# Kernel optimization log

Hardware: AMD Instinct MI355X
Metric: run time of the kernel (lower is better)

Reference implementation:

```python
import jax, jax.numpy as jnp
import numpy as np

GROUPS = 8   # channels // group_size with group_size=8 for C=64
EPS = 1e-5


def group_norm_qc(x0, x1, gamma, beta):
    """LatticeGroupNorm: stats computed jointly over both cosets per (batch, group)."""
    B, C, H, W = x0.shape
    g = GROUPS
    xg = jnp.concatenate([x0.reshape(B, g, -1), x1.reshape(B, g, -1)], axis=-1)
    mean = xg.mean(axis=-1).reshape(B, g, 1, 1, 1)
    var = xg.var(axis=-1).reshape(B, g, 1, 1, 1)
    inv = jax.lax.rsqrt(var + EPS)
    ga = gamma[None, :, None, None]
    be = beta[None, :, None, None]

    def norm(x):
        xr = x.reshape(B, g, C // g, H, W)
        return ((xr - mean) * inv).reshape(B, C, H, W) * ga + be

    return norm(x0), norm(x1)


def qc_conv(x0, x1, w_center, w_corner, bias):
    """Quincunx LatticePad+LatticeConvolution with stencil
    [(0,0),(2,0),(0,2),(2,2),(1,1)], center (1,1).
    w_center: [O,I] tap (1,1) (same-coset 1x1).
    w_corner: [O,I,2,2] taps (0,0),(2,0),(0,2),(2,2) (cross-coset 2x2).
    Pad keeps output cosets the same size as inputs ('same' lattice conv)."""
    dn = ('NCHW', 'OIHW', 'NCHW')

    def c1(x):
        return jnp.einsum('oi,bihw->bohw', w_center, x)

    def c2(x, pad):
        return jax.lax.conv_general_dilated(x, w_corner, (1, 1), pad,
                                            dimension_numbers=dn)

    b = bias[None, :, None, None]
    # coset0 output gathers coset1 at (i-1+a, j-1+b) -> pad top/left
    out0 = c1(x0) + c2(x1, ((1, 0), (1, 0))) + b
    # coset1 output gathers coset0 at (i+a, j+b) -> pad bottom/right
    out1 = c1(x1) + c2(x0, ((0, 1), (0, 1))) + b
    return out0, out1


def setup_inputs() -> dict:
    key = jax.random.key(0)
    ks = jax.random.split(key, 10)
    B, C, H, W = 2, 64, 256, 256
    s = 0.05
    return {
        'x0': jax.random.normal(ks[0], (B, C, H, W), jnp.float32),
        'x1': jax.random.normal(ks[1], (B, C, H, W), jnp.float32),
        'g1': jnp.ones((C,), jnp.float32),
        'b1': jnp.zeros((C,), jnp.float32),
        'w1_center': jax.random.normal(ks[2], (C, C), jnp.float32) * s,
        'w1_corner': jax.random.normal(ks[3], (C, C, 2, 2), jnp.float32) * s,
        'bias1': jax.random.normal(ks[4], (C,), jnp.float32) * s,
        'g2': jnp.ones((C,), jnp.float32),
        'b2': jnp.zeros((C,), jnp.float32),
        'w2_center': jax.random.normal(ks[5], (C, C), jnp.float32) * s,
        'w2_corner': jax.random.normal(ks[6], (C, C, 2, 2), jnp.float32) * s,
        'bias2': jax.random.normal(ks[7], (C,), jnp.float32) * s,
        'w_skip': jax.random.normal(ks[8], (C, C), jnp.float32) * s,
        'bias_skip': jax.random.normal(ks[9], (C,), jnp.float32) * s,
        'g_skip': jnp.ones((C,), jnp.float32),
        'beta_skip': jnp.zeros((C,), jnp.float32),
    }


def reference(x0, x1, g1, b1, w1_center, w1_corner, bias1,
              g2, b2, w2_center, w2_corner, bias2,
              w_skip, bias_skip, g_skip, beta_skip):
    # conv path: GN -> ReLU -> pad+conv -> GN -> ReLU -> pad+conv
    h0, h1 = group_norm_qc(x0, x1, g1, b1)
    h0, h1 = jax.nn.relu(h0), jax.nn.relu(h1)
    h0, h1 = qc_conv(h0, h1, w1_center, w1_corner, bias1)
    h0, h1 = group_norm_qc(h0, h1, g2, b2)
    h0, h1 = jax.nn.relu(h0), jax.nn.relu(h1)
    h0, h1 = qc_conv(h0, h1, w2_center, w2_corner, bias2)
    # skip path: 1x1 lattice conv (stencil [(0,0)]) -> GN
    bsk = bias_skip[None, :, None, None]
    s0 = jnp.einsum('oi,bihw->bohw', w_skip, x0) + bsk
    s1 = jnp.einsum('oi,bihw->bohw', w_skip, x1) + bsk
    s0, s1 = group_norm_qc(s0, s1, g_skip, beta_skip)
    # residual add; stack the two cosets as leading axis for a single output
    return jnp.stack([h0 + s0, h1 + s1])
```

## Files before the change

kernel.cpp:

```cpp
#include <hip/hip_runtime.h>

typedef __attribute__((ext_vector_type(8))) __bf16 bf16x8;
typedef __attribute__((ext_vector_type(4))) __bf16 bf16x4;
typedef __attribute__((ext_vector_type(4))) float f32x4;

#define MFMA16(a,b,c) __builtin_amdgcn_mfma_f32_16x16x32_bf16(a,b,c,0,0,0)

static constexpr int HW = 65536;
static constexpr int WD = 256;
static constexpr int NB = 2;
static constexpr double INV_N = 1.0 / 1048576.0;
static constexpr float EPSV = 1e-5f;

static constexpr size_t OFF_P1  = 0;
static constexpr size_t OFF_P2  = 131072;
static constexpr size_t OFF_A1  = 200704;
static constexpr size_t OFF_A2  = OFF_A1 + 40960;
static constexpr size_t OFF_XT  = OFF_A2 + 40960;
static constexpr size_t SZ_T    = (size_t)2 * NB * HW * 64 * 2;
static constexpr size_t OFF_S   = OFF_XT + SZ_T;
static constexpr size_t OFF_H   = OFF_S + SZ_T;

__global__ __launch_bounds__(256) void K1(
    const float* __restrict__ x0, const float* __restrict__ x1,
    const float* __restrict__ wskip, const float* __restrict__ bskip,
    const float* __restrict__ wc1, const float* __restrict__ wk1,
    const float* __restrict__ wc2, const float* __restrict__ wk2,
    __bf16* __restrict__ xt, __bf16* __restrict__ sout,
    __bf16* __restrict__ A1, __bf16* __restrict__ A2, float* __restrict__ p1) {
  const int bx = blockIdx.x;
  const int t = threadIdx.x;

  if (bx >= 1024) {
    const int stage = bx - 1024;
    const float* wc = stage ? wc2 : wc1;
    const float* wk = stage ? wk2 : wk1;
    __bf16* A = stage ? A2 : A1;
    for (int idx = t; idx < 64 * 320; idx += 256) {
      int o = idx / 320, k = idx - o * 320;
      float v;
      if (k < 64) v = wc[o * 64 + k];
      else {
        int tp = (k - 64) >> 6;
        int c = k & 63;
        v = wk[(o * 64 + c) * 4 + tp];
      }
      A[idx] = (__bf16)v;
    }
    return;
  }

  const int row = bx & 255;
  const int b   = (bx >> 8) & 1;
  const int co  = bx >> 9;
  const float* x = co ? x1 : x0;
  __shared__ __attribute__((aligned(16))) __bf16 tile[256 * 72];
  __shared__ float redp[256];
  __shared__ float reds[32];
  const int wv = t >> 6, lane = t & 63;

  const float* xbase = x + (size_t)b * 64 * HW + (size_t)row * WD + t;
  __bf16* xtbase = xt + (((size_t)(co * NB + b) * HW) + (size_t)row * WD + t) * 64;

  float gsum[8], gsq[8];
#pragma unroll
  for (int g = 0; g < 8; ++g) { gsum[g] = 0.f; gsq[g] = 0.f; }
#pragma unroll
  for (int cg = 0; cg < 8; ++cg) {
    float f[8];
#pragma unroll
    for (int j = 0; j < 8; ++j) f[j] = xbase[(size_t)(cg * 8 + j) * HW];
    bf16x8 v;
#pragma unroll
    for (int j = 0; j < 8; ++j) {
      v[j] = (__bf16)f[j];
      gsum[cg] += f[j];
      gsq[cg] = fmaf(f[j], f[j], gsq[cg]);
    }
    *(bf16x8*)&tile[t * 72 + cg * 8] = v;
    *(bf16x8*)&xtbase[cg * 8] = v;
  }
#pragma unroll
  for (int g = 0; g < 8; ++g) {
#pragma unroll
    for (int m = 1; m < 16; m <<= 1) {
      gsum[g] += __shfl_xor(gsum[g], m, 64);
      gsq[g]  += __shfl_xor(gsq[g], m, 64);
    }
  }
  {
    const int q0 = lane >> 4;
    if ((lane & 15) == 0) {
#pragma unroll
      for (int g = 0; g < 8; ++g) {
        redp[(wv * 4 + q0) * 16 + g] = gsum[g];
        redp[(wv * 4 + q0) * 16 + 8 + g] = gsq[g];
      }
    }
  }
  __syncthreads();

  const int ln = lane & 15, q = lane >> 4;
  const int ch0 = wv * 16 + q * 4;
  bf16x8 a0, a1;
#pragma unroll
  for (int j = 0; j < 8; ++j) {
    a0[j] = (__bf16)wskip[(wv * 16 + ln) * 64 + q * 8 + j];
    a1[j] = (__bf16)wskip[(wv * 16 + ln) * 64 + 32 + q * 8 + j];
  }
  float bia[4];
#pragma unroll
  for (int r = 0; r < 4; ++r) bia[r] = bskip[ch0 + r];

  float ssum = 0.f, ssq = 0.f;
  for (int n = 0; n < 16; ++n) {
    f32x4 acc = {0.f, 0.f, 0.f, 0.f};
    bf16x8 b0 = *(const bf16x8*)&tile[(n * 16 + ln) * 72 + q * 8];
    bf16x8 b1 = *(const bf16x8*)&tile[(n * 16 + ln) * 72 + 32 + q * 8];
    acc = MFMA16(a0, b0, acc);
    acc = MFMA16(a1, b1, acc);
    bf16x4 sv;
    float v[4];
#pragma unroll
    for (int r = 0; r < 4; ++r) {
      v[r] = acc[r] + bia[r];
      ssum += v[r];
      ssq = fmaf(v[r], v[r], ssq);
      sv[r] = (__bf16)v[r];
    }
    size_t sb = ((size_t)(co * NB + b) * 4096 + row * 16 + n) * 1024 + (wv * 4 + q) * 64 + ln * 4;
    *(bf16x4*)&sout[sb] = sv;
  }
#pragma unroll
  for (int m = 1; m < 16; m <<= 1) {
    ssum += __shfl_xor(ssum, m, 64);
    ssq  += __shfl_xor(ssq, m, 64);
  }
  if ((lane & 15) == 0) {
    reds[wv * 4 + q] = ssum;
    reds[16 + wv * 4 + q] = ssq;
  }

  __syncthreads();
  if (t < 32) {
    float val;
    if (t < 16) {
      val = 0.f;
#pragma unroll
      for (int k = 0; k < 16; ++k) val += redp[k * 16 + t];
    } else {
      int kind = (t >> 3) & 1, g = t & 7;
      int wvv = g >> 1, qp = g & 1;
      val = reds[kind * 16 + wvv * 4 + qp * 2] + reds[kind * 16 + wvv * 4 + qp * 2 + 1];
    }
    const int bf1 = (co * 2 + b) * 256 + row;
    p1[(size_t)bf1 * 32 + t] = val;
  }
}

__global__ __launch_bounds__(256) void K2(
    const __bf16* __restrict__ xt, const __bf16* __restrict__ A1,
    const float* __restrict__ p1, const float* __restrict__ g1, const float* __restrict__ be1,
    const float* __restrict__ bias1,
    __bf16* __restrict__ h, float* __restrict__ p2) {
  const int blk = ((blockIdx.x & 7) << 6) | (blockIdx.x >> 3);
  const int tx = blk & 15, ty = blk >> 4;
  const int b = blockIdx.y;
  const int y0p = ty * 8, x0p = tx * 16;
  __shared__ __attribute__((aligned(16))) __bf16 tl[2][153 * 72];
  __shared__ double redn[16];
  __shared__ float sc[64], sh[64];
  __shared__ float lst[16];
  const int t = threadIdx.x;

  {
    const int col = t >> 4, sub = t & 15;
    double v = 0.0;
    for (int j = sub; j < 512; j += 16) {
      int cc = j >> 8, rr = j & 255;
      v += (double)p1[((size_t)(cc * 2 + b) * 256 + rr) * 32 + col];
    }
    v += __shfl_xor(v, 1, 64);
    v += __shfl_xor(v, 2, 64);
    v += __shfl_xor(v, 4, 64);
    v += __shfl_xor(v, 8, 64);
    if (sub == 0) redn[col] = v;
  }
  if (t < 16) lst[t] = 0.f;
  __syncthreads();
  if (t < 64) {
    int g = t >> 3;
    double mean = redn[g] * INV_N;
    double var  = redn[8 + g] * INV_N - mean * mean;
    float inv = rsqrtf((float)var + EPSV);
    float s_ = inv * g1[t];
    sc[t] = s_;
    sh[t] = be1[t] - (float)mean * s_;
  }
  __syncthreads();

#pragma unroll
  for (int i = 0; i < 10; ++i) {
    int u = t + i * 256;
    if (u < 2 * 153 * 8) {
      int cs = u / 1224;
      int rr = u - cs * 1224;
      int px = rr >> 3, cg = rr & 7;
      int ly = px / 17, lx = px - ly * 17;
      int gy = y0p + ly - cs, gx = x0p + lx - cs;
      bf16x8 v;
#pragma unroll
      for (int j = 0; j < 8; ++j) v[j] = (__bf16)0.f;
      if ((unsigned)gy < 256u && (unsigned)gx < 256u) {
        bf16x8 raw = *(const bf16x8*)&xt[(((size_t)(cs * NB + b) * WD + gy) * WD + gx) * 64 + cg * 8];
#pragma unroll
        for (int j = 0; j < 8; ++j) {
          float f = fmaf((float)raw[j], sc[cg * 8 + j], sh[cg * 8 + j]);
          v[j] = (__bf16)fmaxf(f, 0.f);
        }
      }
      *(bf16x8*)&tl[cs][px * 72 + cg * 8] = v;
    }
  }
  __syncthreads();

  const int wv = t >> 6, lane = t & 63, ln = lane & 15, q = lane >> 4;
  const int co = wv & 1, mh = wv >> 1;
  const int q8 = q * 8;
  bf16x8 af[2][10];
#pragma unroll
  for (int m = 0; m < 2; ++m)
#pragma unroll
    for (int kk = 0; kk < 10; ++kk)
      af[m][kk] = *(const bf16x8*)&A1[(mh * 32 + m * 16 + ln) * 320 + kk * 32 + q8];

  f32x4 acc[8][2];
#pragma unroll
  for (int n = 0; n < 8; ++n)
#pragma unroll
    for (int m = 0; m < 2; ++m) acc[n][m] = (f32x4){0.f, 0.f, 0.f, 0.f};

  const __bf16* tc = tl[co];
  const __bf16* to = tl[1 - co];
#pragma unroll
  for (int n = 0; n < 8; ++n) {
    const int cpix = co ? ((n + 1) * 17 + ln + 1) : (n * 17 + ln);
    const int tb = n * 17 + ln;
    const __bf16* pc = tc + cpix * 72 + q8;
    const __bf16* p0 = to + tb * 72 + q8;
    const __bf16* p1p = to + (tb + 1) * 72 + q8;
    const __bf16* p2p = to + (tb + 17) * 72 + q8;
    const __bf16* p3 = to + (tb + 18) * 72 + q8;
    bf16x8 bb;
    bb = *(const bf16x8*)pc;         acc[n][0]=MFMA16(af[0][0],bb,acc[n][0]); acc[n][1]=MFMA16(af[1][0],bb,acc[n][1]);
    bb = *(const bf16x8*)(pc + 32);  acc[n][0]=MFMA16(af[0][1],bb,acc[n][0]); acc[n][1]=MFMA16(af[1][1],bb,acc[n][1]);
    bb = *(const bf16x8*)p0;         acc[n][0]=MFMA16(af[0][2],bb,acc[n][0]); acc[n][1]=MFMA16(af[1][2],bb,acc[n][1]);
    bb = *(const bf16x8*)(p0 + 32);  acc[n][0]=MFMA16(af[0][3],bb,acc[n][0]); acc[n][1]=MFMA16(af[1][3],bb,acc[n][1]);
    bb = *(const bf16x8*)p1p;        acc[n][0]=MFMA16(af[0][4],bb,acc[n][0]); acc[n][1]=MFMA16(af[1][4],bb,acc[n][1]);
    bb = *(const bf16x8*)(p1p + 32); acc[n][0]=MFMA16(af[0][5],bb,acc[n][0]); acc[n][1]=MFMA16(af[1][5],bb,acc[n][1]);
    bb = *(const bf16x8*)p2p;        acc[n][0]=MFMA16(af[0][6],bb,acc[n][0]); acc[n][1]=MFMA16(af[1][6],bb,acc[n][1]);
    bb = *(const bf16x8*)(p2p + 32); acc[n][0]=MFMA16(af[0][7],bb,acc[n][0]); acc[n][1]=MFMA16(af[1][7],bb,acc[n][1]);
    bb = *(const bf16x8*)p3;         acc[n][0]=MFMA16(af[0][8],bb,acc[n][0]); acc[n][1]=MFMA16(af[1][8],bb,acc[n][1]);
    bb = *(const bf16x8*)(p3 + 32);  acc[n][0]=MFMA16(af[0][9],bb,acc[n][0]); acc[n][1]=MFMA16(af[1][9],bb,acc[n][1]);
  }

  __syncthreads();

  float s2s[2] = {0.f, 0.f}, s2q[2] = {0.f, 0.f};
  float bia[2][4];
#pragma unroll
  for (int m = 0; m < 2; ++m)
#pragma unroll
    for (int r = 0; r < 4; ++r) bia[m][r] = bias1[mh * 32 + m * 16 + q * 4 + r];

#pragma unroll
  for (int n = 0; n < 8; ++n)
#pragma unroll
    for (int m = 0; m < 2; ++m) {
      bf16x4 hv;
#pragma unroll
      for (int r = 0; r < 4; ++r) {
        float v = acc[n][m][r] + bia[m][r];
        s2s[m] += v;
        s2q[m] = fmaf(v, v, s2q[m]);
        hv[r] = (__bf16)v;
      }
      *(bf16x4*)&tl[co][(n * 16 + ln) * 72 + mh * 32 + m * 16 + q * 4] = hv;
    }

#pragma unroll
  for (int m = 0; m < 2; ++m) {
    float a_ = s2s[m], c_ = s2q[m];
#pragma unroll
    for (int mk = 1; mk < 32; mk <<= 1) {
      a_ += __shfl_xor(a_, mk, 64);
      c_ += __shfl_xor(c_, mk, 64);
    }
    if ((lane & 31) == 0) {
      int g = mh * 4 + m * 2 + (q >> 1);
      atomicAdd(&lst[g], a_);
      atomicAdd(&lst[8 + g], c_);
    }
  }
  __syncthreads();

#pragma unroll
  for (int i = 0; i < 8; ++i) {
    int co2 = i >> 2;
    int idx = (i & 3) * 256 + t;
    int px = idx >> 3, chunk = idx & 7;
    int gy = y0p + (px >> 4), gx = x0p + (px & 15);
    bf16x8 vv = *(const bf16x8*)&tl[co2][px * 72 + chunk * 8];
    *(bf16x8*)&h[(((size_t)(co2 * NB + b) * WD + gy) * WD + gx) * 64 + chunk * 8] = vv;
  }

  if (t < 16) p2[((size_t)b * 512 + blockIdx.x) * 16 + t] = lst[t];
}

__global__ __launch_bounds__(256) void K3(
    const __bf16* __restrict__ hin, const __bf16* __restrict__ A2,
    const float* __restrict__ p2, const float* __restrict__ p1,
    const float* __restrict__ g2, const float* __restrict__ be2, const float* __restrict__ bias2,
    const float* __restrict__ gsk, const float* __restrict__ besk,
    const __bf16* __restrict__ sin_, float* __restrict__ out) {
  const int blk = ((blockIdx.x & 7) << 6) | (blockIdx.x >> 3);
  const int tx = blk & 15, ty = blk >> 4;
  const int b = blockIdx.y;
  const int y0p = ty * 8, x0p = tx * 16;
  __shared__ __attribute__((aligned(16))) __bf16 tl[2][153 * 72];
  __shared__ double redn[32];
  __shared__ float sc2[64], sh2[64], scS[64], shS[64];
  const int t = threadIdx.x;

  {
    const int col = t >> 3, sub = t & 7;
    double v = 0.0;
    if (col < 16) {
      for (int j = sub; j < 512; j += 8)
        v += (double)p2[((size_t)b * 512 + j) * 16 + col];
    } else {
      for (int j = sub; j < 512; j += 8) {
        int cc = j >> 8, rr = j & 255;
        v += (double)p1[((size_t)(cc * 2 + b) * 256 + rr) * 32 + col];
      }
    }
    v += __shfl_xor(v, 1, 64);
    v += __shfl_xor(v, 2, 64);
    v += __shfl_xor(v, 4, 64);
    if (sub == 0) redn[col] = v;
  }
  __syncthreads();
  if (t < 128) {
    int half = t >> 6, ch = t & 63, g = ch >> 3;
    if (half == 0) {
      double mean = redn[g] * INV_N;
      double var  = redn[8 + g] * INV_N - mean * mean;
      float inv = rsqrtf((float)var + EPSV);
      float s_ = inv * g2[ch];
      sc2[ch] = s_;
      sh2[ch] = be2[ch] - (float)mean * s_;
    } else {
      double mean = redn[16 + g] * INV_N;
      double var  = redn[24 + g] * INV_N - mean * mean;
      float inv = rsqrtf((float)var + EPSV);
      float s_ = inv * gsk[ch];
      scS[ch] = s_;
      shS[ch] = besk[ch] - (float)mean * s_;
    }
  }
  __syncthreads();

#pragma unroll
  for (int i = 0; i < 10; ++i) {
    int u = t + i * 256;
    if (u < 2 * 153 * 8) {
      int cs = u / 1224;
      int rr = u - cs * 1224;
      int px = rr >> 3, cg = rr & 7;
      int ly = px / 17, lx = px - ly * 17;
      int gy = y0p + ly - cs, gx = x0p + lx - cs;
      bf16x8 v;
#pragma unroll
      for (int j = 0; j < 8; ++j) v[j] = (__bf16)0.f;
      if ((unsigned)gy < 256u && (unsigned)gx < 256u) {
        bf16x8 raw = *(const bf16x8*)&hin[(((size_t)(cs * NB + b) * WD + gy) * WD + gx) * 64 + cg * 8];
#pragma unroll
        for (int j = 0; j < 8; ++j) {
          float f = fmaf((float)raw[j], sc2[cg * 8 + j], sh2[cg * 8 + j]);
          v[j] = (__bf16)fmaxf(f, 0.f);
        }
      }
      *(bf16x8*)&tl[cs][px * 72 + cg * 8] = v;
    }
  }
  __syncthreads();

  const int wv = t >> 6, lane = t & 63, ln = lane & 15, q = lane >> 4;
  const int co = wv & 1, mh = wv >> 1;
  const int q8 = q * 8;
  bf16x8 af[2][10];
#pragma unroll
  for (int m = 0; m < 2; ++m)
#pragma unroll
    for (int kk = 0; kk < 10; ++kk)
      af[m][kk] = *(const bf16x8*)&A2[(mh * 32 + m * 16 + ln) * 320 + kk * 32 + q8];

  f32x4 acc[8][2];
#pragma unroll
  for (int n = 0; n < 8; ++n)
#pragma unroll
    for (int m = 0; m < 2; ++m) acc[n][m] = (f32x4){0.f, 0.f, 0.f, 0.f};

  const __bf16* tc = tl[co];
  const __bf16* to = tl[1 - co];
#pragma unroll
  for (int n = 0; n < 8; ++n) {
    const int cpix = co ? ((n + 1) * 17 + ln + 1) : (n * 17 + ln);
    const int tb = n * 17 + ln;
    const __bf16* pc = tc + cpix * 72 + q8;
    const __bf16* p0 = to + tb * 72 + q8;
    const __bf16* p1p = to + (tb + 1) * 72 + q8;
    const __bf16* p2p = to + (tb + 17) * 72 + q8;
    const __bf16* p3 = to + (tb + 18) * 72 + q8;
    bf16x8 bb;
    bb = *(const bf16x8*)pc;         acc[n][0]=MFMA16(af[0][0],bb,acc[n][0]); acc[n][1]=MFMA16(af[1][0],bb,acc[n][1]);
    bb = *(const bf16x8*)(pc + 32);  acc[n][0]=MFMA16(af[0][1],bb,acc[n][0]); acc[n][1]=MFMA16(af[1][1],bb,acc[n][1]);
    bb = *(const bf16x8*)p0;         acc[n][0]=MFMA16(af[0][2],bb,acc[n][0]); acc[n][1]=MFMA16(af[1][2],bb,acc[n][1]);
    bb = *(const bf16x8*)(p0 + 32);  acc[n][0]=MFMA16(af[0][3],bb,acc[n][0]); acc[n][1]=MFMA16(af[1][3],bb,acc[n][1]);
    bb = *(const bf16x8*)p1p;        acc[n][0]=MFMA16(af[0][4],bb,acc[n][0]); acc[n][1]=MFMA16(af[1][4],bb,acc[n][1]);
    bb = *(const bf16x8*)(p1p + 32); acc[n][0]=MFMA16(af[0][5],bb,acc[n][0]); acc[n][1]=MFMA16(af[1][5],bb,acc[n][1]);
    bb = *(const bf16x8*)p2p;        acc[n][0]=MFMA16(af[0][6],bb,acc[n][0]); acc[n][1]=MFMA16(af[1][6],bb,acc[n][1]);
    bb = *(const bf16x8*)(p2p + 32); acc[n][0]=MFMA16(af[0][7],bb,acc[n][0]); acc[n][1]=MFMA16(af[1][7],bb,acc[n][1]);
    bb = *(const bf16x8*)p3;         acc[n][0]=MFMA16(af[0][8],bb,acc[n][0]); acc[n][1]=MFMA16(af[1][8],bb,acc[n][1]);
    bb = *(const bf16x8*)(p3 + 32);  acc[n][0]=MFMA16(af[0][9],bb,acc[n][0]); acc[n][1]=MFMA16(af[1][9],bb,acc[n][1]);
  }

  float bia[2][4], sA[2][4], sB[2][4];
#pragma unroll
  for (int m = 0; m < 2; ++m)
#pragma unroll
    for (int r = 0; r < 4; ++r) {
      int ch = mh * 32 + m * 16 + q * 4 + r;
      bia[m][r] = bias2[ch];
      sA[m][r] = scS[ch];
      sB[m][r] = shS[ch];
    }

#pragma unroll
  for (int n = 0; n < 8; ++n) {
    int gy = y0p + n;
#pragma unroll
    for (int m = 0; m < 2; ++m) {
      int ch0 = mh * 32 + m * 16 + q * 4;
      size_t sb = ((size_t)(co * NB + b) * 4096 + gy * 16 + tx) * 1024 + (mh * 8 + m * 4 + q) * 64 + ln * 4;
      bf16x4 sv = *(const bf16x4*)&sin_[sb];
      size_t ob = ((size_t)(co * NB + b) * 64 + ch0) * HW + (size_t)gy * WD + x0p + ln;
#pragma unroll
      for (int r = 0; r < 4; ++r) {
        float v = acc[n][m][r] + bia[m][r] + fmaf((float)sv[r], sA[m][r], sB[m][r]);
        out[ob + (size_t)r * HW] = v;
      }
    }
  }
}

extern "C" void kernel_launch(void* const* d_in, const int* in_sizes, int n_in,
                              void* d_out, int out_size, void* d_ws, size_t ws_size,
                              hipStream_t stream) {
  (void)in_sizes; (void)n_in; (void)out_size; (void)ws_size;
  const float* x0    = (const float*)d_in[0];
  const float* x1    = (const float*)d_in[1];
  const float* g1    = (const float*)d_in[2];
  const float* b1    = (const float*)d_in[3];
  const float* w1c   = (const float*)d_in[4];
  const float* w1k   = (const float*)d_in[5];
  const float* bias1 = (const float*)d_in[6];
  const float* g2    = (const float*)d_in[7];
  const float* b2    = (const float*)d_in[8];
  const float* w2c   = (const float*)d_in[9];
  const float* w2k   = (const float*)d_in[10];
  const float* bias2 = (const float*)d_in[11];
  const float* wsk   = (const float*)d_in[12];
  const float* bsk   = (const float*)d_in[13];
  const float* gsk   = (const float*)d_in[14];
  const float* besk  = (const float*)d_in[15];

  char* ws = (char*)d_ws;
  float*  p1 = (float*)(ws + OFF_P1);
  float*  p2 = (float*)(ws + OFF_P2);
  __bf16* A1 = (__bf16*)(ws + OFF_A1);
  __bf16* A2 = (__bf16*)(ws + OFF_A2);
  __bf16* xt = (__bf16*)(ws + OFF_XT);
  __bf16* s  = (__bf16*)(ws + OFF_S);
  __bf16* h  = (__bf16*)(ws + OFF_H);

  K1<<<dim3(1026), 256, 0, stream>>>(x0, x1, wsk, bsk, w1c, w1k, w2c, w2k, xt, s, A1, A2, p1);
  K2<<<dim3(512, 2), 256, 0, stream>>>(xt, A1, p1, g1, b1, bias1, h, p2);
  K3<<<dim3(512, 2), 256, 0, stream>>>(h, A2, p2, p1, g2, b2, bias2, gsk, besk, s, (float*)d_out);
}
```

Measured before the change: 294.7 us.

## Hoist GroupNorm stat reductions into tiny kernels and XOR-swizzle LDS tiles

Moves the per-block redundant reduction of partial GroupNorm statistics out of K2/K3 into two small 2-block kernels that write precomputed scale/shift arrays to workspace. Replaces the padded 72-element LDS row stride with a dense 64-element stride plus XOR swizzle, shrinking shared memory and keeping loads bank-conflict free. Adds occupancy hints (launch_bounds 256,4) and overlaps the A-fragment global loads with the tile barrier. It adds two extra kernel launches with their own latency in exchange.

```diff
diff --git a/kernel.cpp b/kernel.cpp
--- a/kernel.cpp
+++ b/kernel.cpp
@@ -14,12 +14,15 @@
 
 static constexpr size_t OFF_P1  = 0;
 static constexpr size_t OFF_P2  = 131072;
+static constexpr size_t OFF_SC  = OFF_P2 + 65536;
 static constexpr size_t OFF_A1  = 200704;
 static constexpr size_t OFF_A2  = OFF_A1 + 40960;
 static constexpr size_t OFF_XT  = OFF_A2 + 40960;
 static constexpr size_t SZ_T    = (size_t)2 * NB * HW * 64 * 2;
 static constexpr size_t OFF_S   = OFF_XT + SZ_T;
 static constexpr size_t OFF_H   = OFF_S + SZ_T;
+
+#define TL8(base, px, c) (*(const bf16x8*)&(base)[(px) * 64 + (((c)) ^ ((((px)) & 7) << 3))])
 
 __global__ __launch_bounds__(256) void K1(
     const float* __restrict__ x0, const float* __restrict__ x1,
@@ -158,45 +161,90 @@
   }
 }
 
-__global__ __launch_bounds__(256) void K2(
+__global__ __launch_bounds__(256) void KR1(
+    const float* __restrict__ p1, const float* __restrict__ g1, const float* __restrict__ be1,
+    const float* __restrict__ gsk, const float* __restrict__ besk, float* __restrict__ scales) {
+  const int b = blockIdx.x;
+  const int t = threadIdx.x;
+  const int col = t >> 3, sub = t & 7;
+  double v = 0.0;
+  for (int j = sub; j < 512; j += 8) {
+    int cc = j >> 8, rr = j & 255;
+    v += (double)p1[((size_t)(cc * 2 + b) * 256 + rr) * 32 + col];
+  }
+  v += __shfl_xor(v, 1, 64);
+  v += __shfl_xor(v, 2, 64);
+  v += __shfl_xor(v, 4, 64);
+  __shared__ double red[32];
+  if (sub == 0) red[col] = v;
+  __syncthreads();
+  if (t < 128) {
+    int half = t >> 6, ch = t & 63, g = ch >> 3;
+    double mean, var;
+    float gm, bt;
+    int kb;
+    if (half == 0) {
+      mean = red[g] * INV_N;
+      var  = red[8 + g] * INV_N - mean * mean;
+      gm = g1[ch]; bt = be1[ch]; kb = 0;
+    } else {
+      mean = red[16 + g] * INV_N;
+      var  = red[24 + g] * INV_N - mean * mean;
+      gm = gsk[ch]; bt = besk[ch]; kb = 2;
+    }
+    float inv = rsqrtf((float)var + EPSV);
+    float s_ = inv * gm;
+    scales[(size_t)kb * 128 + b * 64 + ch] = s_;
+    scales[(size_t)(kb + 1) * 128 + b * 64 + ch] = bt - (float)mean * s_;
+  }
+}
+
+__global__ __launch_bounds__(256) void KR2(
+    const float* __restrict__ p2, const float* __restrict__ g2, const float* __restrict__ be2,
+    float* __restrict__ scales) {
+  const int b = blockIdx.x;
+  const int t = threadIdx.x;
+  const int col = t >> 4, sub = t & 15;
+  double v = 0.0;
+  for (int j = sub; j < 512; j += 16)
+    v += (double)p2[((size_t)b * 512 + j) * 16 + col];
+  v += __shfl_xor(v, 1, 64);
+  v += __shfl_xor(v, 2, 64);
+  v += __shfl_xor(v, 4, 64);
+  v += __shfl_xor(v, 8, 64);
+  __shared__ double red[16];
+  if (sub == 0) red[col] = v;
+  __syncthreads();
+  if (t < 64) {
+    int g = t >> 3;
+    double mean = red[g] * INV_N;
+    double var  = red[8 + g] * INV_N - mean * mean;
+    float inv = rsqrtf((float)var + EPSV);
+    float s_ = inv * g2[t];
+    scales[(size_t)4 * 128 + b * 64 + t] = s_;
+    scales[(size_t)5 * 128 + b * 64 + t] = be2[t] - (float)mean * s_;
+  }
+}
+
+__global__ __launch_bounds__(256, 4) void K2(
     const __bf16* __restrict__ xt, const __bf16* __restrict__ A1,
-    const float* __restrict__ p1, const float* __restrict__ g1, const float* __restrict__ be1,
-    const float* __restrict__ bias1,
+    const float* __restrict__ scales, const float* __restrict__ bias1,
     __bf16* __restrict__ h, float* __restrict__ p2) {
   const int blk = ((blockIdx.x & 7) << 6) | (blockIdx.x >> 3);
   const int tx = blk & 15, ty = blk >> 4;
   const int b = blockIdx.y;
   const int y0p = ty * 8, x0p = tx * 16;
-  __shared__ __attribute__((aligned(16))) __bf16 tl[2][153 * 72];
-  __shared__ double redn[16];
+  __shared__ __attribute__((aligned(16))) __bf16 tl[2][153 * 64];
   __shared__ float sc[64], sh[64];
   __shared__ float lst[16];
   const int t = threadIdx.x;
 
-  {
-    const int col = t >> 4, sub = t & 15;
-    double v = 0.0;
-    for (int j = sub; j < 512; j += 16) {
-      int cc = j >> 8, rr = j & 255;
-      v += (double)p1[((size_t)(cc * 2 + b) * 256 + rr) * 32 + col];
-    }
-    v += __shfl_xor(v, 1, 64);
-    v += __shfl_xor(v, 2, 64);
-    v += __shfl_xor(v, 4, 64);
-    v += __shfl_xor(v, 8, 64);
-    if (sub == 0) redn[col] = v;
+  if (t < 128) {
+    int half = t >> 6, ch = t & 63;
+    float v = scales[(size_t)half * 128 + b * 64 + ch];
+    if (half == 0) sc[ch] = v; else sh[ch] = v;
   }
   if (t < 16) lst[t] = 0.f;
-  __syncthreads();
-  if (t < 64) {
-    int g = t >> 3;
-    double mean = redn[g] * INV_N;
-    double var  = redn[8 + g] * INV_N - mean * mean;
-    float inv = rsqrtf((float)var + EPSV);
-    float s_ = inv * g1[t];
-    sc[t] = s_;
-    sh[t] = be1[t] - (float)mean * s_;
-  }
   __syncthreads();
 
 #pragma unroll
@@ -219,10 +267,9 @@
           v[j] = (__bf16)fmaxf(f, 0.f);
         }
       }
-      *(bf16x8*)&tl[cs][px * 72 + cg * 8] = v;
-    }
-  }
-  __syncthreads();
+      *(bf16x8*)&tl[cs][px * 64 + ((cg ^ (px & 7)) * 8)] = v;
+    }
+  }
 
   const int wv = t >> 6, lane = t & 63, ln = lane & 15, q = lane >> 4;
   const int co = wv & 1, mh = wv >> 1;
@@ -233,6 +280,7 @@
 #pragma unroll
     for (int kk = 0; kk < 10; ++kk)
       af[m][kk] = *(const bf16x8*)&A1[(mh * 32 + m * 16 + ln) * 320 + kk * 32 + q8];
+  __syncthreads();
 
   f32x4 acc[8][2];
 #pragma unroll
@@ -246,22 +294,17 @@
   for (int n = 0; n < 8; ++n) {
     const int cpix = co ? ((n + 1) * 17 + ln + 1) : (n * 17 + ln);
     const int tb = n * 17 + ln;
-    const __bf16* pc = tc + cpix * 72 + q8;
-    const __bf16* p0 = to + tb * 72 + q8;
-    const __bf16* p1p = to + (tb + 1) * 72 + q8;
-    const __bf16* p2p = to + (tb + 17) * 72 + q8;
-    const __bf16* p3 = to + (tb + 18) * 72 + q8;
     bf16x8 bb;
-    bb = *(const bf16x8*)pc;         acc[n][0]=MFMA16(af[0][0],bb,acc[n][0]); acc[n][1]=MFMA16(af[1][0],bb,acc[n][1]);
-    bb = *(const bf16x8*)(pc + 32);  acc[n][0]=MFMA16(af[0][1],bb,acc[n][0]); acc[n][1]=MFMA16(af[1][1],bb,acc[n][1]);
-    bb = *(const bf16x8*)p0;         acc[n][0]=MFMA16(af[0][2],bb,acc[n][0]); acc[n][1]=MFMA16(af[1][2],bb,acc[n][1]);
-    bb = *(const bf16x8*)(p0 + 32);  acc[n][0]=MFMA16(af[0][3],bb,acc[n][0]); acc[n][1]=MFMA16(af[1][3],bb,acc[n][1]);
-    bb = *(const bf16x8*)p1p;        acc[n][0]=MFMA16(af[0][4],bb,acc[n][0]); acc[n][1]=MFMA16(af[1][4],bb,acc[n][1]);
-    bb = *(const bf16x8*)(p1p + 32); acc[n][0]=MFMA16(af[0][5],bb,acc[n][0]); acc[n][1]=MFMA16(af[1][5],bb,acc[n][1]);
-    bb = *(const bf16x8*)p2p;        acc[n][0]=MFMA16(af[0][6],bb,acc[n][0]); acc[n][1]=MFMA16(af[1][6],bb,acc[n][1]);
-    bb = *(const bf16x8*)(p2p + 32); acc[n][0]=MFMA16(af[0][7],bb,acc[n][0]); acc[n][1]=MFMA16(af[1][7],bb,acc[n][1]);
-    bb = *(const bf16x8*)p3;         acc[n][0]=MFMA16(af[0][8],bb,acc[n][0]); acc[n][1]=MFMA16(af[1][8],bb,acc[n][1]);
-    bb = *(const bf16x8*)(p3 + 32);  acc[n][0]=MFMA16(af[0][9],bb,acc[n][0]); acc[n][1]=MFMA16(af[1][9],bb,acc[n][1]);
+    bb = TL8(tc, cpix, q8);          acc[n][0]=MFMA16(af[0][0],bb,acc[n][0]); acc[n][1]=MFMA16(af[1][0],bb,acc[n][1]);
+    bb = TL8(tc, cpix, q8 + 32);     acc[n][0]=MFMA16(af[0][1],bb,acc[n][0]); acc[n][1]=MFMA16(af[1][1],bb,acc[n][1]);
+    bb = TL8(to, tb, q8);            acc[n][0]=MFMA16(af[0][2],bb,acc[n][0]); acc[n][1]=MFMA16(af[1][2],bb,acc[n][1]);
+    bb = TL8(to, tb, q8 + 32);       acc[n][0]=MFMA16(af[0][3],bb,acc[n][0]); acc[n][1]=MFMA16(af[1][3],bb,acc[n][1]);
+    bb = TL8(to, tb + 1, q8);        acc[n][0]=MFMA16(af[0][4],bb,acc[n][0]); acc[n][1]=MFMA16(af[1][4],bb,acc[n][1]);
+    bb = TL8(to, tb + 1, q8 + 32);   acc[n][0]=MFMA16(af[0][5],bb,acc[n][0]); acc[n][1]=MFMA16(af[1][5],bb,acc[n][1]);
+    bb = TL8(to, tb + 17, q8);       acc[n][0]=MFMA16(af[0][6],bb,acc[n][0]); acc[n][1]=MFMA16(af[1][6],bb,acc[n][1]);
+    bb = TL8(to, tb + 17, q8 + 32);  acc[n][0]=MFMA16(af[0][7],bb,acc[n][0]); acc[n][1]=MFMA16(af[1][7],bb,acc[n][1]);
+    bb = TL8(to, tb + 18, q8);       acc[n][0]=MFMA16(af[0][8],bb,acc[n][0]); acc[n][1]=MFMA16(af[1][8],bb,acc[n][1]);
+    bb = TL8(to, tb + 18, q8 + 32);  acc[n][0]=MFMA16(af[0][9],bb,acc[n][0]); acc[n][1]=MFMA16(af[1][9],bb,acc[n][1]);
   }
 
   __syncthreads();
@@ -285,7 +328,7 @@
         s2q[m] = fmaf(v, v, s2q[m]);
         hv[r] = (__bf16)v;
       }
-      *(bf16x4*)&tl[co][(n * 16 + ln) * 72 + mh * 32 + m * 16 + q * 4] = hv;
+      *(bf16x4*)&tl[co][(n * 16 + ln) * 64 + ((mh * 32 + m * 16 + q * 4) ^ ((ln & 7) << 3))] = hv;
     }
 
 #pragma unroll
@@ -310,63 +353,33 @@
     int idx = (i & 3) * 256 + t;
     int px = idx >> 3, chunk = idx & 7;
     int gy = y0p + (px >> 4), gx = x0p + (px & 15);
-    bf16x8 vv = *(const bf16x8*)&tl[co2][px * 72 + chunk * 8];
+    bf16x8 vv = *(const bf16x8*)&tl[co2][px * 64 + ((chunk ^ (px & 7)) * 8)];
     *(bf16x8*)&h[(((size_t)(co2 * NB + b) * WD + gy) * WD + gx) * 64 + chunk * 8] = vv;
   }
 
   if (t < 16) p2[((size_t)b * 512 + blockIdx.x) * 16 + t] = lst[t];
 }
 
-__global__ __launch_bounds__(256) void K3(
+__global__ __launch_bounds__(256, 4) void K3(
     const __bf16* __restrict__ hin, const __bf16* __restrict__ A2,
-    const float* __restrict__ p2, const float* __restrict__ p1,
-    const float* __restrict__ g2, const float* __restrict__ be2, const float* __restrict__ bias2,
-    const float* __restrict__ gsk, const float* __restrict__ besk,
+    const float* __restrict__ scales, const float* __restrict__ bias2,
     const __bf16* __restrict__ sin_, float* __restrict__ out) {
   const int blk = ((blockIdx.x & 7) << 6) | (blockIdx.x >> 3);
   const int tx = blk & 15, ty = blk >> 4;
   const int b = blockIdx.y;
   const int y0p = ty * 8, x0p = tx * 16;
-  __shared__ __attribute__((aligned(16))) __bf16 tl[2][153 * 72];
-  __shared__ double redn[32];
+  __shared__ __attribute__((aligned(16))) __bf16 tl[2][153 * 64];
   __shared__ float sc2[64], sh2[64], scS[64], shS[64];
   const int t = threadIdx.x;
 
   {
-    const int col = t >> 3, sub = t & 7;
-    double v = 0.0;
-    if (col < 16) {
-      for (int j = sub; j < 512; j += 8)
-        v += (double)p2[((size_t)b * 512 + j) * 16 + col];
-    } else {
-      for (int j = sub; j < 512; j += 8) {
-        int cc = j >> 8, rr = j & 255;
-        v += (double)p1[((size_t)(cc * 2 + b) * 256 + rr) * 32 + col];
-      }
-    }
-    v += __shfl_xor(v, 1, 64);
-    v += __shfl_xor(v, 2, 64);
-    v += __shfl_xor(v, 4, 64);
-    if (sub == 0) redn[col] = v;
-  }
-  __syncthreads();
-  if (t < 128) {
-    int half = t >> 6, ch = t & 63, g = ch >> 3;
-    if (half == 0) {
-      double mean = redn[g] * INV_N;
-      double var  = redn[8 + g] * INV_N - mean * mean;
-      float inv = rsqrtf((float)var + EPSV);
-      float s_ = inv * g2[ch];
-      sc2[ch] = s_;
-      sh2[ch] = be2[ch] - (float)mean * s_;
-    } else {
-      double mean = redn[16 + g] * INV_N;
-      double var  = redn[24 + g] * INV_N - mean * mean;
-      float inv = rsqrtf((float)var + EPSV);
-      float s_ = inv * gsk[ch];
-      scS[ch] = s_;
-      shS[ch] = besk[ch] - (float)mean * s_;
-    }
+    int kind = t >> 6, ch = t & 63;
+    int kb = (kind < 2) ? (4 + kind) : kind;
+    float v = scales[(size_t)kb * 128 + b * 64 + ch];
+    if (kind == 0) sc2[ch] = v;
+    else if (kind == 1) sh2[ch] = v;
+    else if (kind == 2) scS[ch] = v;
+    else shS[ch] = v;
   }
   __syncthreads();
 
@@ -390,10 +403,9 @@
           v[j] = (__bf16)fmaxf(f, 0.f);
         }
       }
-      *(bf16x8*)&tl[cs][px * 72 + cg * 8] = v;
-    }
-  }
-  __syncthreads();
+      *(bf16x8*)&tl[cs][px * 64 + ((cg ^ (px & 7)) * 8)] = v;
+    }
+  }
 
   const int wv = t >> 6, lane = t & 63, ln = lane & 15, q = lane >> 4;
   const int co = wv & 1, mh = wv >> 1;
@@ -404,6 +416,7 @@
 #pragma unroll
     for (int kk = 0; kk < 10; ++kk)
       af[m][kk] = *(const bf16x8*)&A2[(mh * 32 + m * 16 + ln) * 320 + kk * 32 + q8];
+  __syncthreads();
 
   f32x4 acc[8][2];
 #pragma unroll
@@ -417,22 +430,17 @@
   for (int n = 0; n < 8; ++n) {
     const int cpix = co ? ((n + 1) * 17 + ln + 1) : (n * 17 + ln);
     const int tb = n * 17 + ln;
-    const __bf16* pc = tc + cpix * 72 + q8;
-    const __bf16* p0 = to + tb * 72 + q8;
-    const __bf16* p1p = to + (tb + 1) * 72 + q8;
-    const __bf16* p2p = to + (tb + 17) * 72 + q8;
-    const __bf16* p3 = to + (tb + 18) * 72 + q8;
     bf16x8 bb;
-    bb = *(const bf16x8*)pc;         acc[n][0]=MFMA16(af[0][0],bb,acc[n][0]); acc[n][1]=MFMA16(af[1][0],bb,acc[n][1]);
-    bb = *(const bf16x8*)(pc + 32);  acc[n][0]=MFMA16(af[0][1],bb,acc[n][0]); acc[n][1]=MFMA16(af[1][1],bb,acc[n][1]);
-    bb = *(const bf16x8*)p0;         acc[n][0]=MFMA16(af[0][2],bb,acc[n][0]); acc[n][1]=MFMA16(af[1][2],bb,acc[n][1]);
-    bb = *(const bf16x8*)(p0 + 32);  acc[n][0]=MFMA16(af[0][3],bb,acc[n][0]); acc[n][1]=MFMA16(af[1][3],bb,acc[n][1]);
-    bb = *(const bf16x8*)p1p;        acc[n][0]=MFMA16(af[0][4],bb,acc[n][0]); acc[n][1]=MFMA16(af[1][4],bb,acc[n][1]);
-    bb = *(const bf16x8*)(p1p + 32); acc[n][0]=MFMA16(af[0][5],bb,acc[n][0]); acc[n][1]=MFMA16(af[1][5],bb,acc[n][1]);
-    bb = *(const bf16x8*)p2p;        acc[n][0]=MFMA16(af[0][6],bb,acc[n][0]); acc[n][1]=MFMA16(af[1][6],bb,acc[n][1]);
-    bb = *(const bf16x8*)(p2p + 32); acc[n][0]=MFMA16(af[0][7],bb,acc[n][0]); acc[n][1]=MFMA16(af[1][7],bb,acc[n][1]);
-    bb = *(const bf16x8*)p3;         acc[n][0]=MFMA16(af[0][8],bb,acc[n][0]); acc[n][1]=MFMA16(af[1][8],bb,acc[n][1]);
-    bb = *(const bf16x8*)(p3 + 32);  acc[n][0]=MFMA16(af[0][9],bb,acc[n][0]); acc[n][1]=MFMA16(af[1][9],bb,acc[n][1]);
+    bb = TL8(tc, cpix, q8);          acc[n][0]=MFMA16(af[0][0],bb,acc[n][0]); acc[n][1]=MFMA16(af[1][0],bb,acc[n][1]);
+    bb = TL8(tc, cpix, q8 + 32);     acc[n][0]=MFMA16(af[0][1],bb,acc[n][0]); acc[n][1]=MFMA16(af[1][1],bb,acc[n][1]);
+    bb = TL8(to, tb, q8);            acc[n][0]=MFMA16(af[0][2],bb,acc[n][0]); acc[n][1]=MFMA16(af[1][2],bb,acc[n][1]);
+    bb = TL8(to, tb, q8 + 32);       acc[n][0]=MFMA16(af[0][3],bb,acc[n][0]); acc[n][1]=MFMA16(af[1][3],bb,acc[n][1]);
+    bb = TL8(to, tb + 1, q8);        acc[n][0]=MFMA16(af[0][4],bb,acc[n][0]); acc[n][1]=MFMA16(af[1][4],bb,acc[n][1]);
+    bb = TL8(to, tb + 1, q8 + 32);   acc[n][0]=MFMA16(af[0][5],bb,acc[n][0]); acc[n][1]=MFMA16(af[1][5],bb,acc[n][1]);
+    bb = TL8(to, tb + 17, q8);       acc[n][0]=MFMA16(af[0][6],bb,acc[n][0]); acc[n][1]=MFMA16(af[1][6],bb,acc[n][1]);
+    bb = TL8(to, tb + 17, q8 + 32);  acc[n][0]=MFMA16(af[0][7],bb,acc[n][0]); acc[n][1]=MFMA16(af[1][7],bb,acc[n][1]);
+    bb = TL8(to, tb + 18, q8);       acc[n][0]=MFMA16(af[0][8],bb,acc[n][0]); acc[n][1]=MFMA16(af[1][8],bb,acc[n][1]);
+    bb = TL8(to, tb + 18, q8 + 32);  acc[n][0]=MFMA16(af[0][9],bb,acc[n][0]); acc[n][1]=MFMA16(af[1][9],bb,acc[n][1]);
   }
 
   float bia[2][4], sA[2][4], sB[2][4];
@@ -488,6 +496,7 @@
   char* ws = (char*)d_ws;
   float*  p1 = (float*)(ws + OFF_P1);
   float*  p2 = (float*)(ws + OFF_P2);
+  float*  scl= (float*)(ws + OFF_SC);
   __bf16* A1 = (__bf16*)(ws + OFF_A1);
   __bf16* A2 = (__bf16*)(ws + OFF_A2);
   __bf16* xt = (__bf16*)(ws + OFF_XT);
@@ -495,6 +504,8 @@
   __bf16* h  = (__bf16*)(ws + OFF_H);
 
   K1<<<dim3(1026), 256, 0, stream>>>(x0, x1, wsk, bsk, w1c, w1k, w2c, w2k, xt, s, A1, A2, p1);
-  K2<<<dim3(512, 2), 256, 0, stream>>>(xt, A1, p1, g1, b1, bias1, h, p2);
-  K3<<<dim3(512, 2), 256, 0, stream>>>(h, A2, p2, p1, g2, b2, bias2, gsk, besk, s, (float*)d_out);
+  KR1<<<dim3(2), 256, 0, stream>>>(p1, g1, b1, gsk, besk, scl);
+  K2<<<dim3(512, 2), 256, 0, stream>>>(xt, A1, scl, bias1, h, p2);
+  KR2<<<dim3(2), 256, 0, stream>>>(p2, g2, b2, scl);
+  K3<<<dim3(512, 2), 256, 0, stream>>>(h, A2, scl, bias2, s, (float*)d_out);
 }
```

Result: slower. 309.7 us (+5.1%).
